# Kernel tuning notes

Measured on AMD Instinct MI355X. Metric: run time of the kernel, lower is better.

The kernel has to match this reference:

```python
import jax, jax.numpy as jnp
import numpy as np

B, C, D, H, W = 8, 256, 128, 64, 64


def setup_inputs() -> dict:
    key = jax.random.key(0)
    ks = jax.random.split(key, 7)
    s = 1.0 / np.sqrt(C)
    return {
        "q": jax.random.normal(ks[0], (B, C, H, W), dtype=jnp.float32),
        "k": jax.random.normal(ks[1], (B, C, H, W), dtype=jnp.float32),
        "v": jax.random.normal(ks[2], (B, C, H, W), dtype=jnp.float32),
        "W_theta": jax.random.normal(ks[3], (D, C), dtype=jnp.float32) * s,
        "W_phi": jax.random.normal(ks[4], (D, C), dtype=jnp.float32) * s,
        "W_g": jax.random.normal(ks[5], (D, C), dtype=jnp.float32) * s,
        "W_out": jax.random.normal(ks[6], (C, D), dtype=jnp.float32) * (1.0 / np.sqrt(D)),
    }


def reference(q, k, v, W_theta, W_phi, W_g, W_out):
    # 1x1 conv projections (no bias) == channel matmuls
    b, c, h, w = q.shape
    d = W_theta.shape[0]
    n = h * w
    qp = jnp.einsum('bchw,dc->bhwd', q, W_theta).reshape(b, n, d)   # [B,N,d]
    kp = jnp.einsum('bchw,dc->bhwd', k, W_phi).reshape(b, n, d)     # [B,N,d]
    vp = jnp.einsum('bchw,dc->bhwd', v, W_g).reshape(b, n, d)       # [B,N,d]
    # embedded_gaussian: scores / sqrt(d), softmax over dim=1 (query axis!)
    scores = jnp.einsum('bnd,bmd->bnm', qp, kp) / jnp.sqrt(jnp.asarray(d, qp.dtype))
    attn = jax.nn.softmax(scores, axis=1)                           # NOTE: axis=1, matches torch dim=1
    out = jnp.einsum('bnm,bmd->bnd', attn, vp).reshape(b, h, w, d)  # [B,H,W,d]
    out = jnp.einsum('bhwd,cd->bchw', out, W_out)                   # conv_out 1x1
    return v + out
```

## Files before the change

kernel.cpp:

```cpp
#include <hip/hip_runtime.h>
#include <stdint.h>

#define B_ 8
#define C_ 256
#define D_ 128
#define N_ 4096

typedef __bf16 bf16x8 __attribute__((ext_vector_type(8)));
typedef uint16_t u16x8 __attribute__((ext_vector_type(8)));
typedef uint16_t u16x4 __attribute__((ext_vector_type(4)));
typedef float f32x4 __attribute__((ext_vector_type(4)));
typedef uint32_t u32x2 __attribute__((ext_vector_type(2)));

__device__ inline uint16_t f2bf(float x) {
    union { float f; uint32_t u; } v; v.f = x;
    uint32_t u = v.u;
    return (uint16_t)((u + 0x7FFFu + ((u >> 16) & 1u)) >> 16);
}

__device__ inline float bf2f(uint16_t v) {
    union { uint32_t u; float f; } x; x.u = (uint32_t)v << 16; return x.f;
}

__device__ inline uint32_t pkbf(float lo, float hi) {
    __bf16 l = (__bf16)lo, h = (__bf16)hi;
    uint16_t lu = __builtin_bit_cast(uint16_t, l);
    uint16_t hu = __builtin_bit_cast(uint16_t, h);
    return ((uint32_t)hu << 16) | (uint32_t)lu;
}

__device__ inline float dexp2(float x) { return __builtin_amdgcn_exp2f(x); }

__global__ __launch_bounds__(256) void prep_weights(
    const float* __restrict__ wt, const float* __restrict__ wp,
    const float* __restrict__ wg, const float* __restrict__ wo,
    uint16_t* __restrict__ bwt, uint16_t* __restrict__ bwp,
    uint16_t* __restrict__ bwg, uint16_t* __restrict__ bwo)
{
    int i = blockIdx.x * 256 + threadIdx.x;
    const float scale = 0.127517431f;
    bwt[i] = f2bf(wt[i] * scale);
    bwp[i] = f2bf(wp[i]);
    bwg[i] = f2bf(wg[i]);
    bwo[i] = f2bf(wo[i]);
}

__global__ __launch_bounds__(256) void proj_kernel(
    const float* __restrict__ q, const float* __restrict__ k, const float* __restrict__ v,
    const uint16_t* __restrict__ bwt, const uint16_t* __restrict__ bwp, const uint16_t* __restrict__ bwg,
    uint16_t* __restrict__ qp, uint16_t* __restrict__ kp, uint16_t* __restrict__ vpT)
{
    const int b = blockIdx.x & 7;
    const int rest = blockIdx.x >> 3;
    const int which = rest >> 6;
    const int n0 = (rest & 63) * 64;
    const float* src = (which == 0) ? q : ((which == 1) ? k : v);
    const uint16_t* w = (which == 0) ? bwt : ((which == 1) ? bwp : bwg);
    const int wav = threadIdx.x >> 6;
    const int lane = threadIdx.x & 63;
    const int col = lane & 15;
    const int quad = lane >> 4;
    const int n = n0 + wav * 16 + col;

    const float* srcb = src + (size_t)b * C_ * N_;

    f32x4 acc[8];
#pragma unroll
    for (int mf = 0; mf < 8; ++mf) acc[mf] = (f32x4){0.f, 0.f, 0.f, 0.f};

#pragma unroll
    for (int kc = 0; kc < 8; ++kc) {
        const int cbase = kc * 32 + quad * 8;
        bf16x8 afr[8];
#pragma unroll
        for (int mf = 0; mf < 8; ++mf)
            afr[mf] = *(const bf16x8*)(w + (size_t)(mf * 16 + col) * C_ + cbase);
        float x[8];
#pragma unroll
        for (int j = 0; j < 8; ++j)
            x[j] = srcb[(size_t)(cbase + j) * N_ + n];
        u32x2 blo = (u32x2){pkbf(x[0], x[1]), pkbf(x[2], x[3])};
        u32x2 bhi = (u32x2){pkbf(x[4], x[5]), pkbf(x[6], x[7])};
        uint32_t bw[4] = {blo[0], blo[1], bhi[0], bhi[1]};
        bf16x8 bfrag = __builtin_bit_cast(bf16x8, bw);
#pragma unroll
        for (int mf = 0; mf < 8; ++mf)
            acc[mf] = __builtin_amdgcn_mfma_f32_16x16x32_bf16(afr[mf], bfrag, acc[mf], 0, 0, 0);
    }

    if (which < 2) {
        uint16_t* dst = (which == 0) ? qp : kp;
        uint16_t* base = dst + ((size_t)b * N_ + n) * D_;
#pragma unroll
        for (int mf = 0; mf < 8; ++mf) {
            u32x2 pk = (u32x2){pkbf(acc[mf][0], acc[mf][1]), pkbf(acc[mf][2], acc[mf][3])};
            *(u32x2*)(base + mf * 16 + quad * 4) = pk;
        }
    } else {
        uint16_t* base = vpT + (size_t)b * D_ * N_;
#pragma unroll
        for (int mf = 0; mf < 8; ++mf)
#pragma unroll
            for (int r = 0; r < 4; ++r) {
                int d = mf * 16 + quad * 4 + r;
                base[(size_t)d * N_ + n] = f2bf(acc[mf][r]);
            }
    }
}

__global__ __launch_bounds__(256) void pass1_denom(
    const uint16_t* __restrict__ qp, const uint16_t* __restrict__ kp,
    float* __restrict__ part)
{
    const int b  = blockIdx.x & 7;
    const int mt = (blockIdx.x >> 3) & 31;
    const int ns = blockIdx.x >> 8;
    const int m0 = mt * 128;
    const int wav = threadIdx.x >> 6;
    const int lane = threadIdx.x & 63;
    const int c = lane & 15;
    const int q = lane >> 4;

    const uint16_t* qpb = qp + (size_t)b * N_ * D_;
    const uint16_t* kpb = kp + (size_t)b * N_ * D_;

    bf16x8 bfr[8][4];
#pragma unroll
    for (int mf = 0; mf < 8; ++mf)
#pragma unroll
        for (int kc = 0; kc < 4; ++kc)
            bfr[mf][kc] = *(const bf16x8*)(kpb + (size_t)(m0 + mf * 16 + c) * D_ + kc * 32 + q * 8);

    float colsum[8];
#pragma unroll
    for (int mf = 0; mf < 8; ++mf) colsum[mf] = 0.f;

#define P1_LOAD(AFR, IT)                                                          \
    {   const int nbase = ns * 2048 + (IT) * 64 + wav * 16;                       \
        _Pragma("unroll")                                                         \
        for (int kc = 0; kc < 4; ++kc)                                            \
            AFR[kc] = *(const bf16x8*)(qpb + (size_t)(nbase + c) * D_ + kc * 32 + q * 8); }

#define P1_COMPUTE(AFR)                                                           \
    {   _Pragma("unroll")                                                         \
        for (int mf = 0; mf < 8; ++mf) {                                          \
            f32x4 acc = (f32x4){0.f, 0.f, 0.f, 0.f};                              \
            _Pragma("unroll")                                                     \
            for (int kc = 0; kc < 4; ++kc)                                        \
                acc = __builtin_amdgcn_mfma_f32_16x16x32_bf16(AFR[kc], bfr[mf][kc], acc, 0, 0, 0); \
            _Pragma("unroll")                                                     \
            for (int r = 0; r < 4; ++r) colsum[mf] += dexp2(acc[r]);              \
        } }

    bf16x8 afrA[4], afrB[4];
    P1_LOAD(afrA, 0);
    for (int it2 = 0; it2 < 16; ++it2) {
        P1_LOAD(afrB, 2 * it2 + 1);
        P1_COMPUTE(afrA);
        if (it2 < 15) P1_LOAD(afrA, 2 * it2 + 2);
        P1_COMPUTE(afrB);
    }
#undef P1_LOAD
#undef P1_COMPUTE

    __shared__ float cs[4][128];
#pragma unroll
    for (int mf = 0; mf < 8; ++mf) {
        float s = colsum[mf];
        s += __shfl_down(s, 16, 64);
        s += __shfl_down(s, 32, 64);
        if (q == 0) cs[wav][mf * 16 + c] = s;
    }
    __syncthreads();
    if (threadIdx.x < 128) {
        float s = cs[0][threadIdx.x] + cs[1][threadIdx.x] + cs[2][threadIdx.x] + cs[3][threadIdx.x];
        part[((size_t)ns * 8 + b) * N_ + m0 + threadIdx.x] = s;
    }
}

__global__ __launch_bounds__(256) void neglog2_kernel(
    const float* __restrict__ part, float* __restrict__ l2i)
{
    const int b  = blockIdx.x & 7;
    const int m0 = (blockIdx.x >> 3) * 256;
    const int i = b * N_ + m0 + threadIdx.x;
    l2i[i] = -__builtin_amdgcn_logf(part[i] + part[8 * N_ + i]);
}

__global__ __launch_bounds__(256, 2) void pass2_attn(
    const uint16_t* __restrict__ qp, const uint16_t* __restrict__ kp,
    const uint16_t* __restrict__ vpT, const float* __restrict__ l2i,
    uint16_t* __restrict__ ob0, uint16_t* __restrict__ ob1,
    uint16_t* __restrict__ ob2, uint16_t* __restrict__ ob3)
{
    const int b   = blockIdx.x & 7;
    const int qtr = (blockIdx.x >> 3) & 3;
    const int nsb = blockIdx.x >> 5;
    const int wav = threadIdx.x >> 6;
    const int lane = threadIdx.x & 63;
    const int c = lane & 15;
    const int q = lane >> 4;
    const int ntile = nsb * 256 + wav * 64;

    const uint16_t* qpb = qp + (size_t)b * N_ * D_;
    const uint16_t* kpb = kp + (size_t)b * N_ * D_;
    const uint16_t* vtb = vpT + (size_t)b * D_ * N_;
    const float* l2b = l2i + (size_t)b * N_;

    __shared__ __align__(16) uint16_t stage[2][8192];
    __shared__ __align__(16) uint16_t plds[4][4][16][72];

#define STAGE(bufidx, m0_)                                                          \
    {                                                                               \
        uint16_t* lb = &stage[bufidx][0];                                           \
        _Pragma("unroll")                                                           \
        for (int j = 0; j < 4; ++j) {                                               \
            const int fid = wav * 4 + j;                                            \
            const uint16_t* g;                                                      \
            uint16_t* ld;                                                           \
            if (fid < 8) {                                                          \
                const int P = fid * 64 + lane;                                      \
                const int mm = P >> 4, js = P & 15;                                 \
                const int jj = js ^ (mm & 7);                                       \
                g = kpb + (size_t)((m0_) + mm) * D_ + jj * 8;                       \
                ld = lb + fid * 512;                                                \
            } else {                                                                \
                const int P = (fid - 8) * 64 + lane;                                \
                const int dd = P >> 2, js = P & 3;                                  \
                const int jj = js ^ ((dd >> 1) & 3);                                \
                g = vtb + (size_t)dd * N_ + (m0_) + jj * 8;                         \
                ld = lb + 4096 + (fid - 8) * 512;                                   \
            }                                                                       \
            __builtin_amdgcn_global_load_lds(                                       \
                (const __attribute__((address_space(1))) unsigned int*)g,           \
                (__attribute__((address_space(3))) unsigned int*)ld,                \
                16, 0, 0);                                                          \
        }                                                                           \
    }

    bf16x8 qfr[4][4];
#pragma unroll
    for (int nf = 0; nf < 4; ++nf)
#pragma unroll
        for (int kc = 0; kc < 4; ++kc)
            qfr[nf][kc] = *(const bf16x8*)(qpb + (size_t)(ntile + nf * 16 + c) * D_ + kc * 32 + q * 8);

    f32x4 oacc[4][8];
#pragma unroll
    for (int nf = 0; nf < 4; ++nf)
#pragma unroll
        for (int df = 0; df < 8; ++df) oacc[nf][df] = (f32x4){0.f, 0.f, 0.f, 0.f};

    const int mstart = qtr * (N_ / 4);
    STAGE(0, mstart);
    __syncthreads();

    for (int ch = 0; ch < 32; ++ch) {
        const int m0 = mstart + ch * 32;
        const int cur = ch & 1;
        if (ch < 31) STAGE(cur ^ 1, m0 + 32);

        const uint16_t* sb = &stage[cur][0];

        const f32x4 bias0 = *(const f32x4*)(l2b + m0 + 4 * q);
        const f32x4 bias1 = *(const f32x4*)(l2b + m0 + 16 + 4 * q);

        bf16x8 kf[2][4];
#pragma unroll
        for (int mf = 0; mf < 2; ++mf)
#pragma unroll
            for (int kc = 0; kc < 4; ++kc) {
                const int js = (kc * 4 + q) ^ (c & 7);
                kf[mf][kc] = *(const bf16x8*)(sb + (mf * 16 + c) * 128 + js * 8);
            }

        __builtin_amdgcn_s_setprio(1);
#pragma unroll
        for (int nf = 0; nf < 4; ++nf) {
            f32x4 s0 = bias0;
            f32x4 s1 = bias1;
#pragma unroll
            for (int kc = 0; kc < 4; ++kc)
                s0 = __builtin_amdgcn_mfma_f32_16x16x32_bf16(kf[0][kc], qfr[nf][kc], s0, 0, 0, 0);
#pragma unroll
            for (int kc = 0; kc < 4; ++kc)
                s1 = __builtin_amdgcn_mfma_f32_16x16x32_bf16(kf[1][kc], qfr[nf][kc], s1, 0, 0, 0);
            uint32_t p00 = pkbf(dexp2(s0[0]), dexp2(s0[1]));
            uint32_t p01 = pkbf(dexp2(s0[2]), dexp2(s0[3]));
            uint32_t p10 = pkbf(dexp2(s1[0]), dexp2(s1[1]));
            uint32_t p11 = pkbf(dexp2(s1[2]), dexp2(s1[3]));
            uint16_t* row = &plds[wav][nf][c][0];
            *(u32x2*)(row + 4 * q)      = (u32x2){p00, p01};
            *(u32x2*)(row + 16 + 4 * q) = (u32x2){p10, p11};
        }
        __builtin_amdgcn_s_setprio(0);

        const int vjs = q ^ ((c >> 1) & 3);
        bf16x8 vf[8];
#pragma unroll
        for (int df = 0; df < 8; ++df)
            vf[df] = *(const bf16x8*)(sb + 4096 + (df * 16 + c) * 32 + vjs * 8);

        bf16x8 pf[4];
#pragma unroll
        for (int nf = 0; nf < 4; ++nf)
            pf[nf] = *(const bf16x8*)(&plds[wav][nf][c][8 * q]);

        __builtin_amdgcn_s_setprio(1);
#pragma unroll
        for (int nf = 0; nf < 4; ++nf)
#pragma unroll
            for (int df = 0; df < 8; ++df)
                oacc[nf][df] = __builtin_amdgcn_mfma_f32_16x16x32_bf16(pf[nf], vf[df], oacc[nf][df], 0, 0, 0);
        __builtin_amdgcn_s_setprio(0);

        __syncthreads();
    }
#undef STAGE

    uint16_t* obq = (qtr == 0) ? ob0 : (qtr == 1) ? ob1 : (qtr == 2) ? ob2 : ob3;
#pragma unroll
    for (int nf = 0; nf < 4; ++nf) {
        uint16_t* ob = obq + ((size_t)b * N_ + ntile + nf * 16) * D_;
#pragma unroll
        for (int df = 0; df < 8; ++df)
#pragma unroll
            for (int r = 0; r < 4; ++r)
                ob[(size_t)(q * 4 + r) * D_ + df * 16 + c] = f2bf(oacc[nf][df][r]);
    }
}

__global__ __launch_bounds__(256) void pass3_out(
    const uint16_t* __restrict__ ob0, const uint16_t* __restrict__ ob1,
    const uint16_t* __restrict__ ob2, const uint16_t* __restrict__ ob3,
    const uint16_t* __restrict__ bwo,
    const float* __restrict__ v, float* __restrict__ out)
{
    const int b  = blockIdx.x & 7;
    const int n0 = (blockIdx.x >> 3) * 64;
    const int wav = threadIdx.x >> 6;
    const int lane = threadIdx.x & 63;
    const int col = lane & 15;
    const int quad = lane >> 4;
    const int n = n0 + wav * 16 + col;

    const float* vb = v + (size_t)b * C_ * N_;
    float* outb = out + (size_t)b * C_ * N_;
    const size_t off = ((size_t)b * N_ + n) * D_;

    bf16x8 f0[4], f1[4], f2[4], f3[4];
#pragma unroll
    for (int kc = 0; kc < 4; ++kc) {
        f0[kc] = *(const bf16x8*)(ob0 + off + kc * 32 + quad * 8);
        f1[kc] = *(const bf16x8*)(ob1 + off + kc * 32 + quad * 8);
        f2[kc] = *(const bf16x8*)(ob2 + off + kc * 32 + quad * 8);
        f3[kc] = *(const bf16x8*)(ob3 + off + kc * 32 + quad * 8);
    }

#pragma unroll
    for (int cf = 0; cf < 16; ++cf) {
        f32x4 acc = (f32x4){0.f, 0.f, 0.f, 0.f};
#pragma unroll
        for (int kc = 0; kc < 4; ++kc) {
            bf16x8 afr = *(const bf16x8*)(bwo + (size_t)(cf * 16 + col) * D_ + kc * 32 + quad * 8);
            acc = __builtin_amdgcn_mfma_f32_16x16x32_bf16(afr, f0[kc], acc, 0, 0, 0);
            acc = __builtin_amdgcn_mfma_f32_16x16x32_bf16(afr, f1[kc], acc, 0, 0, 0);
            acc = __builtin_amdgcn_mfma_f32_16x16x32_bf16(afr, f2[kc], acc, 0, 0, 0);
            acc = __builtin_amdgcn_mfma_f32_16x16x32_bf16(afr, f3[kc], acc, 0, 0, 0);
        }
#pragma unroll
        for (int r = 0; r < 4; ++r) {
            const int cc = cf * 16 + quad * 4 + r;
            const size_t idx = (size_t)cc * N_ + n;
            outb[idx] = vb[idx] + acc[r];
        }
    }
}

extern "C" void kernel_launch(void* const* d_in, const int* in_sizes, int n_in,
                              void* d_out, int out_size, void* d_ws, size_t ws_size,
                              hipStream_t stream) {
    const float* q  = (const float*)d_in[0];
    const float* k  = (const float*)d_in[1];
    const float* v  = (const float*)d_in[2];
    const float* wt = (const float*)d_in[3];
    const float* wp = (const float*)d_in[4];
    const float* wg = (const float*)d_in[5];
    const float* wo = (const float*)d_in[6];
    float* out = (float*)d_out;

    const size_t PROJ = (size_t)B_ * N_ * D_;
    uint16_t* qp  = (uint16_t*)d_ws;
    uint16_t* kp  = qp + PROJ;
    uint16_t* vpT = kp + PROJ;
    uint16_t* ob0 = vpT + PROJ;
    uint16_t* ob1 = ob0 + PROJ;
    uint16_t* ob2 = ob1 + PROJ;
    uint16_t* ob3 = ob2 + PROJ;
    uint16_t* bwt = ob3 + PROJ;
    uint16_t* bwp = bwt + (size_t)D_ * C_;
    uint16_t* bwg = bwp + (size_t)D_ * C_;
    uint16_t* bwo = bwg + (size_t)D_ * C_;
    float* part   = (float*)(bwo + (size_t)D_ * C_);
    float* l2i    = part + (size_t)2 * 8 * N_;

    prep_weights<<<dim3(128), 256, 0, stream>>>(wt, wp, wg, wo, bwt, bwp, bwg, bwo);
    proj_kernel<<<dim3(1536), 256, 0, stream>>>(q, k, v, bwt, bwp, bwg, qp, kp, vpT);
    pass1_denom<<<dim3(512), 256, 0, stream>>>(qp, kp, part);
    neglog2_kernel<<<dim3(128), 256, 0, stream>>>(part, l2i);
    pass2_attn<<<dim3(512), 256, 0, stream>>>(qp, kp, vpT, l2i, ob0, ob1, ob2, ob3);
    pass3_out<<<dim3(512), 256, 0, stream>>>(ob0, ob1, ob2, ob3, bwo, v, out);
}
```

Baseline: 374.6 us.

## Fold log-normalizer into pass1 and pre-sum partial outputs in pass3

pass1_denom now runs 512-thread blocks that each cover 64 key columns over the full query range. It reduces across 8 waves in shared memory and writes the negative log of the column sum directly, which removes the separate neglog2 kernel and the partial-sum buffer. pass3_out adds the four bf16 partial attention outputs elementwise in fp32 and repacks the sum to bf16, then runs one MFMA per k-chunk instead of four. In exchange, each pass1 block streams twice as many query rows, and the summed partial output goes through one more bf16 rounding.

```diff
diff --git a/kernel.cpp b/kernel.cpp
--- a/kernel.cpp
+++ b/kernel.cpp
@@ -108,14 +108,13 @@
     }
 }
 
-__global__ __launch_bounds__(256) void pass1_denom(
+__global__ __launch_bounds__(512, 4) void pass1_denom(
     const uint16_t* __restrict__ qp, const uint16_t* __restrict__ kp,
-    float* __restrict__ part)
+    float* __restrict__ l2i)
 {
     const int b  = blockIdx.x & 7;
-    const int mt = (blockIdx.x >> 3) & 31;
-    const int ns = blockIdx.x >> 8;
-    const int m0 = mt * 128;
+    const int mt = blockIdx.x >> 3;
+    const int m0 = mt * 64;
     const int wav = threadIdx.x >> 6;
     const int lane = threadIdx.x & 63;
     const int c = lane & 15;
@@ -124,26 +123,26 @@
     const uint16_t* qpb = qp + (size_t)b * N_ * D_;
     const uint16_t* kpb = kp + (size_t)b * N_ * D_;
 
-    bf16x8 bfr[8][4];
-#pragma unroll
-    for (int mf = 0; mf < 8; ++mf)
+    bf16x8 bfr[4][4];
+#pragma unroll
+    for (int mf = 0; mf < 4; ++mf)
 #pragma unroll
         for (int kc = 0; kc < 4; ++kc)
             bfr[mf][kc] = *(const bf16x8*)(kpb + (size_t)(m0 + mf * 16 + c) * D_ + kc * 32 + q * 8);
 
-    float colsum[8];
-#pragma unroll
-    for (int mf = 0; mf < 8; ++mf) colsum[mf] = 0.f;
+    float colsum[4];
+#pragma unroll
+    for (int mf = 0; mf < 4; ++mf) colsum[mf] = 0.f;
 
 #define P1_LOAD(AFR, IT)                                                          \
-    {   const int nbase = ns * 2048 + (IT) * 64 + wav * 16;                       \
+    {   const int nbase = (IT) * 128 + wav * 16;                                  \
         _Pragma("unroll")                                                         \
         for (int kc = 0; kc < 4; ++kc)                                            \
             AFR[kc] = *(const bf16x8*)(qpb + (size_t)(nbase + c) * D_ + kc * 32 + q * 8); }
 
 #define P1_COMPUTE(AFR)                                                           \
     {   _Pragma("unroll")                                                         \
-        for (int mf = 0; mf < 8; ++mf) {                                          \
+        for (int mf = 0; mf < 4; ++mf) {                                          \
             f32x4 acc = (f32x4){0.f, 0.f, 0.f, 0.f};                              \
             _Pragma("unroll")                                                     \
             for (int kc = 0; kc < 4; ++kc)                                        \
@@ -163,28 +162,21 @@
 #undef P1_LOAD
 #undef P1_COMPUTE
 
-    __shared__ float cs[4][128];
-#pragma unroll
-    for (int mf = 0; mf < 8; ++mf) {
+    __shared__ float cs[8][64];
+#pragma unroll
+    for (int mf = 0; mf < 4; ++mf) {
         float s = colsum[mf];
         s += __shfl_down(s, 16, 64);
         s += __shfl_down(s, 32, 64);
         if (q == 0) cs[wav][mf * 16 + c] = s;
     }
     __syncthreads();
-    if (threadIdx.x < 128) {
-        float s = cs[0][threadIdx.x] + cs[1][threadIdx.x] + cs[2][threadIdx.x] + cs[3][threadIdx.x];
-        part[((size_t)ns * 8 + b) * N_ + m0 + threadIdx.x] = s;
-    }
-}
-
-__global__ __launch_bounds__(256) void neglog2_kernel(
-    const float* __restrict__ part, float* __restrict__ l2i)
-{
-    const int b  = blockIdx.x & 7;
-    const int m0 = (blockIdx.x >> 3) * 256;
-    const int i = b * N_ + m0 + threadIdx.x;
-    l2i[i] = -__builtin_amdgcn_logf(part[i] + part[8 * N_ + i]);
+    if (threadIdx.x < 64) {
+        float s = 0.f;
+#pragma unroll
+        for (int wv = 0; wv < 8; ++wv) s += cs[wv][threadIdx.x];
+        l2i[(size_t)b * N_ + m0 + threadIdx.x] = -__builtin_amdgcn_logf(s);
+    }
 }
 
 __global__ __launch_bounds__(256, 2) void pass2_attn(
@@ -348,13 +340,20 @@
     float* outb = out + (size_t)b * C_ * N_;
     const size_t off = ((size_t)b * N_ + n) * D_;
 
-    bf16x8 f0[4], f1[4], f2[4], f3[4];
+    bf16x8 fs[4];
 #pragma unroll
     for (int kc = 0; kc < 4; ++kc) {
-        f0[kc] = *(const bf16x8*)(ob0 + off + kc * 32 + quad * 8);
-        f1[kc] = *(const bf16x8*)(ob1 + off + kc * 32 + quad * 8);
-        f2[kc] = *(const bf16x8*)(ob2 + off + kc * 32 + quad * 8);
-        f3[kc] = *(const bf16x8*)(ob3 + off + kc * 32 + quad * 8);
+        u16x8 a0 = *(const u16x8*)(ob0 + off + kc * 32 + quad * 8);
+        u16x8 a1 = *(const u16x8*)(ob1 + off + kc * 32 + quad * 8);
+        u16x8 a2 = *(const u16x8*)(ob2 + off + kc * 32 + quad * 8);
+        u16x8 a3 = *(const u16x8*)(ob3 + off + kc * 32 + quad * 8);
+        float s[8];
+#pragma unroll
+        for (int j = 0; j < 8; ++j)
+            s[j] = bf2f(a0[j]) + bf2f(a1[j]) + bf2f(a2[j]) + bf2f(a3[j]);
+        uint32_t w4[4] = {pkbf(s[0], s[1]), pkbf(s[2], s[3]),
+                          pkbf(s[4], s[5]), pkbf(s[6], s[7])};
+        fs[kc] = __builtin_bit_cast(bf16x8, w4);
     }
 
 #pragma unroll
@@ -363,10 +362,7 @@
 #pragma unroll
         for (int kc = 0; kc < 4; ++kc) {
             bf16x8 afr = *(const bf16x8*)(bwo + (size_t)(cf * 16 + col) * D_ + kc * 32 + quad * 8);
-            acc = __builtin_amdgcn_mfma_f32_16x16x32_bf16(afr, f0[kc], acc, 0, 0, 0);
-            acc = __builtin_amdgcn_mfma_f32_16x16x32_bf16(afr, f1[kc], acc, 0, 0, 0);
-            acc = __builtin_amdgcn_mfma_f32_16x16x32_bf16(afr, f2[kc], acc, 0, 0, 0);
-            acc = __builtin_amdgcn_mfma_f32_16x16x32_bf16(afr, f3[kc], acc, 0, 0, 0);
+            acc = __builtin_amdgcn_mfma_f32_16x16x32_bf16(afr, fs[kc], acc, 0, 0, 0);
         }
 #pragma unroll
         for (int r = 0; r < 4; ++r) {
@@ -401,13 +397,11 @@
     uint16_t* bwp = bwt + (size_t)D_ * C_;
     uint16_t* bwg = bwp + (size_t)D_ * C_;
     uint16_t* bwo = bwg + (size_t)D_ * C_;
-    float* part   = (float*)(bwo + (size_t)D_ * C_);
-    float* l2i    = part + (size_t)2 * 8 * N_;
+    float* l2i    = (float*)(bwo + (size_t)D_ * C_);
 
     prep_weights<<<dim3(128), 256, 0, stream>>>(wt, wp, wg, wo, bwt, bwp, bwg, bwo);
     proj_kernel<<<dim3(1536), 256, 0, stream>>>(q, k, v, bwt, bwp, bwg, qp, kp, vpT);
-    pass1_denom<<<dim3(512), 256, 0, stream>>>(qp, kp, part);
-    neglog2_kernel<<<dim3(128), 256, 0, stream>>>(part, l2i);
+    pass1_denom<<<dim3(512), 512, 0, stream>>>(qp, kp, l2i);
     pass2_attn<<<dim3(512), 256, 0, stream>>>(qp, kp, vpT, l2i, ob0, ob1, ob2, ob3);
     pass3_out<<<dim3(512), 256, 0, stream>>>(ob0, ob1, ob2, ob3, bwo, v, out);
 }
```

New measurement: 394.5 us. 5.3% more time.
